# Performance work log

Measured on AMD Instinct MI355X. Metric: run time of the kernel, lower is better.

Reference implementation:

```python
import jax, jax.numpy as jnp
import numpy as np

# Sizes (match init_kwargs / input_specs)
N, D, H, E = 4096, 512, 2048, 8   # tokens, dim, hidden_dim, num_experts
DK = 2                             # dynamic_k = top_k(3) - fixed_k(1)
NC = E - 1                         # dynamic candidate count (experts 1..7)
BETA_FIXED = 1.0 / 3.0             # fixed_k / top_k
BETA_DYN = 2.0 / 3.0               # dynamic_k / top_k


def setup_inputs() -> dict:
    key = jax.random.key(0)
    ks = jax.random.split(key, 5)
    def init(k, shape, fan_in):
        return jax.random.normal(k, shape, jnp.float32) * (1.0 / np.sqrt(fan_in))
    return {
        "x": jax.random.normal(ks[0], (N, D), jnp.float32),
        "router_W": init(ks[1], (D, NC), D),      # Linear(dim, num_non_fixed)
        "router_b": jnp.zeros((NC,), jnp.float32),
        "W1": init(ks[2], (E, D, H), D),           # per-expert first Linear
        "b1": jnp.zeros((E, H), jnp.float32),
        "W2": init(ks[3], (E, H, D), H),           # per-expert second Linear
        "b2": jnp.zeros((E, D), jnp.float32),
        "fixed_w": jnp.ones((1,), jnp.float32),    # fixed_branch_weights
    }


def reference(x, router_W, router_b, W1, b1, W2, b2, fixed_w):
    # All-expert MLP computed once (dense grouped-GEMM form of the
    # per-expert gather/MLP/scatter loop in the torch module).
    h = jax.nn.relu(jnp.einsum("nd,edh->neh", x, W1) + b1)   # [N,E,H]
    y = jnp.einsum("neh,ehd->ned", h, W2) + b2               # [N,E,D]

    # Fixed branch: expert 0 with fixed weight.
    fixed_out = fixed_w[0] * y[:, 0]                          # [N,D]

    # Dynamic branch: router over the 7 non-fixed experts.
    logits = x @ router_W + router_b                          # [N,NC]
    top_logits, top_idx = jax.lax.top_k(logits, DK)           # [N,DK]
    gates = jax.nn.softmax(top_logits, axis=-1)               # [N,DK]
    sel_expert = top_idx + 1                                  # lookup non_fixed [1..7]

    # combine weights per (token, expert): scatter gates via one-hot.
    combine = jnp.sum(jax.nn.one_hot(sel_expert, E, dtype=x.dtype)
                      * gates[..., None], axis=1)             # [N,E]
    dyn_out = jnp.einsum("ned,ne->nd", y, combine)            # [N,D]

    mixed = BETA_FIXED * fixed_out + BETA_DYN * dyn_out

    # Aux losses (same math as torch).
    importance = jax.nn.softmax(logits, axis=-1).mean(axis=0)  # [NC]
    uniform = 1.0 / NC
    load_balance_loss = jnp.mean((importance - uniform) ** 2)
    router_entropy = -jnp.sum(importance * jnp.log(jnp.clip(importance, 1e-8)))

    return mixed, load_balance_loss, router_entropy, sel_expert
```

## Files before the change

### kernel.cpp

```cpp
#include <hip/hip_runtime.h>
#include <math.h>

#define N_TOK 4096
#define DIM   512
#define HID   2048
#define NEXP  8
#define NC    7
#define OUT_MIXED (N_TOK*DIM)
#define TM    48
#define TPE   86

typedef __attribute__((ext_vector_type(8))) short bf16x8;
typedef __attribute__((ext_vector_type(4))) float f32x4;

#define XSP 520
#define HSP 136

#define OFF_TOK  4096ull
#define OFF_WT   (OFF_TOK + 131072ull)
#define OFF_XBF  (OFF_WT + 131072ull)
#define OFF_W1S  (OFF_XBF + 4194304ull)
#define OFF_W2S  (OFF_W1S + 16777216ull)
#define WS_REQ   (OFF_W2S + 16777216ull)

__device__ inline unsigned short f2bf(float f) {
  unsigned int u = __builtin_bit_cast(unsigned int, f);
  u = (u + 0x7fffu + ((u >> 16) & 1u)) >> 16;
  return (unsigned short)u;
}

__device__ void dev_convert_w(const float* __restrict__ W,
                              unsigned int* __restrict__ Ws,
                              int K, int Nm, int tiles_n, int b,
                              unsigned short (*lds)[264])
{
  const int tid = threadIdx.x;
  const int e  = b >> 7;
  const int rm = b & 127;
  const int tk = rm / tiles_n;
  const int tn = rm - tk * tiles_n;

  const float* src = W + ((size_t)e * K + tk * 32) * Nm + tn * 256;
#pragma unroll
  for (int it = 0; it < 8; ++it) {
    const int g   = it * 256 + tid;
    const int row = g >> 6, c4 = g & 63;
    const float4 v = *(const float4*)(src + (size_t)row * Nm + c4 * 4);
    ushort4 o;
    o.x = f2bf(v.x); o.y = f2bf(v.y); o.z = f2bf(v.z); o.w = f2bf(v.w);
    *(ushort4*)(&lds[row][c4 * 4]) = o;
  }
  __syncthreads();

  const int ntiles = Nm >> 4, kblks = K >> 3;
#pragma unroll
  for (int it = 0; it < 16; ++it) {
    const int uid   = it * 256 + tid;
    const int nt_l  = uid >> 8;
    const int r     = uid & 255;
    const int kb_l  = r >> 6;
    const int u     = r & 63;
    const int n_lo  = u >> 2;
    const int k_hf  = u & 3;
    const int d_l   = kb_l * 8 + k_hf * 2;
    const int h_l   = nt_l * 16 + n_lo;
    const unsigned int s0 = lds[d_l][h_l], s1 = lds[d_l + 1][h_l];
    const int nt_g = tn * 16 + nt_l;
    const int kb_g = tk * 4 + kb_l;
    const size_t frag = ((size_t)e * ntiles + nt_g) * kblks + kb_g;
    Ws[frag * 64 + n_lo * 4 + k_hf] = s0 | (s1 << 16);
  }
}

__global__ __launch_bounds__(256) void prep_kernel(
    const float* __restrict__ x, const float* __restrict__ rW,
    const float* __restrict__ rb,
    const float* __restrict__ W1, const float* __restrict__ W2,
    float* __restrict__ out,
    int* __restrict__ cpad, float* __restrict__ ipad, int* __restrict__ done,
    int* __restrict__ tok_list, float* __restrict__ wt_list,
    unsigned short* __restrict__ xbf,
    unsigned int* __restrict__ W1s, unsigned int* __restrict__ W2s)
{
  __shared__ unsigned short clds[32][264];
  __shared__ float imp_loc[8];
  __shared__ int   cnt_loc[8];
  __shared__ int   ltok[8][32];
  __shared__ float lwt[8][32];
  __shared__ int   base_s[8];

  const int tid = threadIdx.x;
  const int blk = blockIdx.x;

  if (blk >= 256) {
    const int b = blk - 256;
    if (b < 512) {
      float* p = out + ((size_t)b * 256 + tid) * 16;
      const float4 z = {0.f, 0.f, 0.f, 0.f};
      *(float4*)(p)      = z;  *(float4*)(p + 4)  = z;
      *(float4*)(p + 8)  = z;  *(float4*)(p + 12) = z;
    } else if (b < 1536) {
      const int g = (b - 512) * 256 + tid;
      const float* src = x + (size_t)g * 8;
      unsigned short tmp[8];
#pragma unroll
      for (int j = 0; j < 8; ++j) tmp[j] = f2bf(src[j]);
      *(uint4*)(xbf + (size_t)g * 8) = *(const uint4*)tmp;
    } else if (b < 2560) {
      dev_convert_w(W1, W1s, DIM, HID, 8, b - 1536, clds);
    } else {
      dev_convert_w(W2, W2s, HID, DIM, 2, b - 2560, clds);
    }
    return;
  }

  if (tid < 8) { imp_loc[tid] = 0.f; cnt_loc[tid] = 0; }
  __syncthreads();
  const int wave = tid >> 6, lane = tid & 63;

  float rw[2][4][NC];
#pragma unroll
  for (int j = 0; j < 2; ++j) {
    const float* p = rW + j * 1792 + lane * 28;
    float tmp[28];
#pragma unroll
    for (int u = 0; u < 7; ++u) *(float4*)(tmp + u * 4) = *(const float4*)(p + u * 4);
#pragma unroll
    for (int k = 0; k < 4; ++k)
#pragma unroll
      for (int e = 0; e < NC; ++e) rw[j][k][e] = tmp[k * 7 + e];
  }

  for (int it = 0; it < 4; ++it) {
    const int t = blk * 16 + wave * 4 + it;
    const float4 xa = *(const float4*)(x + (size_t)t * DIM + lane * 4);
    const float4 xb = *(const float4*)(x + (size_t)t * DIM + 256 + lane * 4);
    const float xv[2][4] = {{xa.x, xa.y, xa.z, xa.w}, {xb.x, xb.y, xb.z, xb.w}};
    float lg[NC];
#pragma unroll
    for (int e = 0; e < NC; ++e) {
      float s = 0.f;
#pragma unroll
      for (int j = 0; j < 2; ++j)
#pragma unroll
        for (int k = 0; k < 4; ++k) s += xv[j][k] * rw[j][k][e];
      lg[e] = s;
    }
#pragma unroll
    for (int e = 0; e < NC; ++e) {
      float s = lg[e];
#pragma unroll
      for (int off = 32; off > 0; off >>= 1) s += __shfl_xor(s, off, 64);
      lg[e] = s + rb[e];
    }
    int i1 = 0; float l1 = lg[0];
#pragma unroll
    for (int e = 1; e < NC; ++e) { if (lg[e] > l1) { l1 = lg[e]; i1 = e; } }
    int i2 = -1; float l2 = -3.4e38f;
#pragma unroll
    for (int e = 0; e < NC; ++e) { if (e != i1 && lg[e] > l2) { l2 = lg[e]; i2 = e; } }

    const float ed = expf(l2 - l1);
    const float g1 = 1.f/(1.f+ed), g2 = ed/(1.f+ed);

    float p[NC]; float ssum = 0.f;
#pragma unroll
    for (int e = 0; e < NC; ++e) { p[e] = expf(lg[e] - l1); ssum += p[e]; }
    const float inv = 1.f/ssum;

    if (lane == 0) {
#pragma unroll
      for (int e = 0; e < NC; ++e) atomicAdd(&imp_loc[e], p[e]*inv);
      out[OUT_MIXED + 2 + 2*t]     = (float)(i1 + 1);
      out[OUT_MIXED + 2 + 2*t + 1] = (float)(i2 + 1);
      const int e1 = i1 + 1, e2 = i2 + 1;
      int p1 = atomicAdd(&cnt_loc[e1], 1);
      ltok[e1][p1] = t;  lwt[e1][p1] = (2.f/3.f)*g1;
      int p2 = atomicAdd(&cnt_loc[e2], 1);
      ltok[e2][p2] = t;  lwt[e2][p2] = (2.f/3.f)*g2;
    }
  }
  __syncthreads();

  if (tid >= 1 && tid < 8)
    base_s[tid] = atomicAdd(&cpad[tid * 32], cnt_loc[tid]);
  if (tid < NC)
    atomicAdd(&ipad[(tid + 1) * 32], imp_loc[tid]);
  __syncthreads();

  {
    const int e = tid >> 5, i = tid & 31;
    if (e >= 1 && i < cnt_loc[e]) {
      const int dst = e * N_TOK + base_s[e] + i;
      tok_list[dst] = ltok[e][i];
      wt_list [dst] = lwt[e][i];
    }
  }

  if (tid == 0) {
    __threadfence();
    const int old = atomicAdd(done, 1);
    if (old == 255) {
      __threadfence();
      float lb = 0.f, ent = 0.f;
      for (int e = 0; e < NC; ++e) {
        float p = ipad[(e + 1) * 32] * (1.f/(float)N_TOK);
        float d = p - (1.f/(float)NC);
        lb += d*d;
        ent -= p * logf(fmaxf(p, 1e-8f));
      }
      out[OUT_MIXED]     = lb * (1.f/(float)NC);
      out[OUT_MIXED + 1] = ent;
    }
  }
}

__global__ __launch_bounds__(512, 4) void moe_mlp_mfma(
    const unsigned short* __restrict__ xbf,
    const unsigned short* __restrict__ W1s,
    const unsigned short* __restrict__ W2s,
    const float* __restrict__ b1, const float* __restrict__ b2,
    const float* __restrict__ fixed_w,
    const int* __restrict__ cpad, const int* __restrict__ tok_list,
    const float* __restrict__ wt_list, float* __restrict__ out)
{
  const int e    = blockIdx.x / (TPE * 2);
  const int r    = blockIdx.x % (TPE * 2);
  const int tile = r >> 1;
  const int half = r & 1;
  const int cnt  = (e == 0) ? N_TOK : cpad[e * 32];
  const int start = tile * TM;
  if (start >= cnt) return;

  __shared__ __align__(16) unsigned short xs[TM * XSP];
  __shared__ __align__(16) unsigned short hs[TM * HSP];
  __shared__ int   tok_s[TM];
  __shared__ float wt_s[TM];

  const int tid = threadIdx.x;
  if (tid < TM) {
    int idx = start + tid; int t = 0; float w = 0.f;
    if (idx < cnt) {
      if (e == 0) { t = idx; w = (1.f/3.f) * fixed_w[0]; }
      else        { t = tok_list[e*N_TOK + idx]; w = wt_list[e*N_TOK + idx]; }
    }
    tok_s[tid] = t; wt_s[tid] = w;
  }
  __syncthreads();

  for (int i = tid; i < TM * 64; i += 512) {
    const int m = i >> 6, cb = i & 63;
    *(uint4*)(xs + m * XSP + cb * 8) =
        *(const uint4*)(xbf + (size_t)tok_s[m] * DIM + cb * 8);
  }

  const int lane = tid & 63;
  const int w    = tid >> 6;
  const int l15  = lane & 15;
  const int q    = lane >> 4;

  const unsigned short* W1e = W1s + (size_t)e * 128 * 64 * 128;
  const unsigned short* W2e = W2s + (size_t)e * 32 * 256 * 128;

  f32x4 yacc[3][4];
#pragma unroll
  for (int mi = 0; mi < 3; ++mi)
#pragma unroll
    for (int t = 0; t < 4; ++t) yacc[mi][t] = (f32x4){0.f, 0.f, 0.f, 0.f};

  __syncthreads();

  for (int c = half * 8; c < half * 8 + 8; ++c) {
    const int nt = c * 8 + w;
    f32x4 hacc[3];
#pragma unroll
    for (int mi = 0; mi < 3; ++mi) hacc[mi] = (f32x4){0.f, 0.f, 0.f, 0.f};
#pragma unroll 4
    for (int s = 0; s < 16; ++s) {
      const bf16x8 a0 = *(const bf16x8*)(xs + l15 * XSP + s * 32 + q * 8);
      const bf16x8 a1 = *(const bf16x8*)(xs + (16 + l15) * XSP + s * 32 + q * 8);
      const bf16x8 a2 = *(const bf16x8*)(xs + (32 + l15) * XSP + s * 32 + q * 8);
      const bf16x8 b = *(const bf16x8*)(
          W1e + ((size_t)nt * 64 + s * 4 + q) * 128 + l15 * 8);
      hacc[0] = __builtin_amdgcn_mfma_f32_16x16x32_bf16(a0, b, hacc[0], 0, 0, 0);
      hacc[1] = __builtin_amdgcn_mfma_f32_16x16x32_bf16(a1, b, hacc[1], 0, 0, 0);
      hacc[2] = __builtin_amdgcn_mfma_f32_16x16x32_bf16(a2, b, hacc[2], 0, 0, 0);
    }
    {
      const float bv = b1[e * HID + nt * 16 + l15];
      const int col = w * 16 + l15;
#pragma unroll
      for (int mi = 0; mi < 3; ++mi)
#pragma unroll
        for (int reg = 0; reg < 4; ++reg)
          hs[(mi * 16 + q * 4 + reg) * HSP + col] =
              f2bf(fmaxf(hacc[mi][reg] + bv, 0.f));
    }
    __syncthreads();

#pragma unroll
    for (int s = 0; s < 4; ++s) {
      const bf16x8 a0 = *(const bf16x8*)(hs + l15 * HSP + s * 32 + q * 8);
      const bf16x8 a1 = *(const bf16x8*)(hs + (16 + l15) * HSP + s * 32 + q * 8);
      const bf16x8 a2 = *(const bf16x8*)(hs + (32 + l15) * HSP + s * 32 + q * 8);
      const int kblk = c * 16 + s * 4 + q;
#pragma unroll
      for (int t = 0; t < 4; ++t) {
        const bf16x8 b = *(const bf16x8*)(
            W2e + (((size_t)(w * 4 + t) * 256) + kblk) * 128 + l15 * 8);
        yacc[0][t] = __builtin_amdgcn_mfma_f32_16x16x32_bf16(a0, b, yacc[0][t], 0, 0, 0);
        yacc[1][t] = __builtin_amdgcn_mfma_f32_16x16x32_bf16(a1, b, yacc[1][t], 0, 0, 0);
        yacc[2][t] = __builtin_amdgcn_mfma_f32_16x16x32_bf16(a2, b, yacc[2][t], 0, 0, 0);
      }
    }
    __syncthreads();
  }

#pragma unroll
  for (int t = 0; t < 4; ++t) {
    const int d = (w * 4 + t) * 16 + l15;
    const float b2v = half ? 0.f : b2[e * DIM + d];
#pragma unroll
    for (int mi = 0; mi < 3; ++mi)
#pragma unroll
      for (int reg = 0; reg < 4; ++reg) {
        const int m = mi * 16 + q * 4 + reg;
        atomicAdd(&out[(size_t)tok_s[m] * DIM + d], wt_s[m] * (yacc[mi][t][reg] + b2v));
      }
  }
}

__global__ __launch_bounds__(256) void router_only(
    const float* __restrict__ x, const float* __restrict__ rW,
    const float* __restrict__ rb, float* __restrict__ out,
    int* __restrict__ cpad, float* __restrict__ ipad, int* __restrict__ done,
    int* __restrict__ tok_list, float* __restrict__ wt_list)
{
  __shared__ float imp_loc[8];
  __shared__ int   cnt_loc[8];
  __shared__ int   ltok[8][32];
  __shared__ float lwt[8][32];
  __shared__ int   base_s[8];

  const int tid = threadIdx.x;
  if (tid < 8) { imp_loc[tid] = 0.f; cnt_loc[tid] = 0; }
  __syncthreads();
  const int wave = tid >> 6, lane = tid & 63;

  for (int it = 0; it < 4; ++it) {
    const int t = blockIdx.x * 16 + wave * 4 + it;
    float xv[8];
#pragma unroll
    for (int j = 0; j < 8; ++j) xv[j] = x[(size_t)t*DIM + lane + 64*j];
    float lg[NC];
#pragma unroll
    for (int e = 0; e < NC; ++e) {
      float s = 0.f;
#pragma unroll
      for (int j = 0; j < 8; ++j) s += xv[j] * rW[(lane + 64*j)*NC + e];
      lg[e] = s;
    }
#pragma unroll
    for (int e = 0; e < NC; ++e) {
      float s = lg[e];
#pragma unroll
      for (int off = 32; off > 0; off >>= 1) s += __shfl_xor(s, off, 64);
      lg[e] = s + rb[e];
    }
    int i1 = 0; float l1 = lg[0];
#pragma unroll
    for (int e = 1; e < NC; ++e) { if (lg[e] > l1) { l1 = lg[e]; i1 = e; } }
    int i2 = -1; float l2 = -3.4e38f;
#pragma unroll
    for (int e = 0; e < NC; ++e) { if (e != i1 && lg[e] > l2) { l2 = lg[e]; i2 = e; } }
    const float ed = expf(l2 - l1);
    const float g1 = 1.f/(1.f+ed), g2 = ed/(1.f+ed);
    float p[NC]; float ssum = 0.f;
#pragma unroll
    for (int e = 0; e < NC; ++e) { p[e] = expf(lg[e] - l1); ssum += p[e]; }
    const float inv = 1.f/ssum;
    if (lane == 0) {
#pragma unroll
      for (int e = 0; e < NC; ++e) atomicAdd(&imp_loc[e], p[e]*inv);
      out[OUT_MIXED + 2 + 2*t]     = (float)(i1 + 1);
      out[OUT_MIXED + 2 + 2*t + 1] = (float)(i2 + 1);
      const int e1 = i1 + 1, e2 = i2 + 1;
      int p1 = atomicAdd(&cnt_loc[e1], 1);
      ltok[e1][p1] = t;  lwt[e1][p1] = (2.f/3.f)*g1;
      int p2 = atomicAdd(&cnt_loc[e2], 1);
      ltok[e2][p2] = t;  lwt[e2][p2] = (2.f/3.f)*g2;
    }
  }
  __syncthreads();
  if (tid >= 1 && tid < 8)
    base_s[tid] = atomicAdd(&cpad[tid * 32], cnt_loc[tid]);
  if (tid < NC)
    atomicAdd(&ipad[(tid + 1) * 32], imp_loc[tid]);
  __syncthreads();
  {
    const int e = tid >> 5, i = tid & 31;
    if (e >= 1 && i < cnt_loc[e]) {
      const int dst = e * N_TOK + base_s[e] + i;
      tok_list[dst] = ltok[e][i];
      wt_list [dst] = lwt[e][i];
    }
  }
  if (tid == 0) {
    __threadfence();
    const int old = atomicAdd(done, 1);
    if (old == 255) {
      __threadfence();
      float lb = 0.f, ent = 0.f;
      for (int e = 0; e < NC; ++e) {
        float p = ipad[(e + 1) * 32] * (1.f/(float)N_TOK);
        float d = p - (1.f/(float)NC);
        lb += d*d;
        ent -= p * logf(fmaxf(p, 1e-8f));
      }
      out[OUT_MIXED]     = lb * (1.f/(float)NC);
      out[OUT_MIXED + 1] = ent;
    }
  }
}

__global__ __launch_bounds__(256) void moe_mlp_kernel(
    const float* __restrict__ x,
    const float* __restrict__ W1, const float* __restrict__ b1,
    const float* __restrict__ W2, const float* __restrict__ b2,
    const float* __restrict__ fixed_w,
    const int* __restrict__ cpad, const int* __restrict__ tok_list,
    const float* __restrict__ wt_list, float* __restrict__ out)
{
  const int e    = blockIdx.x >> 8;
  const int tile = blockIdx.x & 255;
  const int cnt  = (e == 0) ? N_TOK : cpad[e * 32];
  const int start = tile * 16;
  if (start >= cnt) return;

  __shared__ float xs[DIM][17];
  __shared__ float hs2[256][17];
  __shared__ int   tok_s[16];
  __shared__ float wt_s[16];

  const int tid = threadIdx.x;
  if (tid < 16) {
    int idx = start + tid; int t = 0; float w = 0.f;
    if (idx < cnt) {
      if (e == 0) { t = idx; w = (1.f/3.f) * fixed_w[0]; }
      else        { t = tok_list[e*N_TOK + idx]; w = wt_list[e*N_TOK + idx]; }
    }
    tok_s[tid] = t; wt_s[tid] = w;
  }
  __syncthreads();

  for (int i = tid; i < 16*DIM; i += 256) {
    const int m = i >> 9, d = i & (DIM-1);
    xs[d][m] = x[(size_t)tok_s[m]*DIM + d];
  }

  const int r  = tid & 63;
  const int m0 = (tid >> 6) * 4;
  const float* W1e = W1 + (size_t)e * DIM * HID;
  const float* W2e = W2 + (size_t)e * HID * DIM;
  const float* b1e = b1 + e * HID;

  float yacc[4][8];
#pragma unroll
  for (int j = 0; j < 4; ++j)
#pragma unroll
    for (int i = 0; i < 8; ++i) yacc[j][i] = 0.f;

  __syncthreads();

  for (int c = 0; c < 8; ++c) {
    const int k0 = c * 256;
    float bv[4];
#pragma unroll
    for (int i = 0; i < 4; ++i) bv[i] = b1e[k0 + r + 64*i];
    float hacc[4][4];
#pragma unroll
    for (int j = 0; j < 4; ++j)
#pragma unroll
      for (int i = 0; i < 4; ++i) hacc[j][i] = bv[i];
#pragma unroll 2
    for (int d = 0; d < DIM; ++d) {
      float wv[4];
#pragma unroll
      for (int i = 0; i < 4; ++i) wv[i] = W1e[(size_t)d*HID + k0 + r + 64*i];
      float xv[4];
#pragma unroll
      for (int j = 0; j < 4; ++j) xv[j] = xs[d][m0+j];
#pragma unroll
      for (int j = 0; j < 4; ++j)
#pragma unroll
        for (int i = 0; i < 4; ++i) hacc[j][i] += xv[j]*wv[i];
    }
#pragma unroll
    for (int i = 0; i < 4; ++i)
#pragma unroll
      for (int j = 0; j < 4; ++j) hs2[r + 64*i][m0+j] = fmaxf(hacc[j][i], 0.f);
    __syncthreads();

#pragma unroll 2
    for (int k = 0; k < 256; ++k) {
      float wv2[8];
#pragma unroll
      for (int i = 0; i < 8; ++i) wv2[i] = W2e[(size_t)(k0+k)*DIM + r + 64*i];
      float hv[4];
#pragma unroll
      for (int j = 0; j < 4; ++j) hv[j] = hs2[k][m0+j];
#pragma unroll
      for (int j = 0; j < 4; ++j)
#pragma unroll
        for (int i = 0; i < 8; ++i) yacc[j][i] += hv[j]*wv2[i];
    }
    __syncthreads();
  }

#pragma unroll
  for (int i = 0; i < 8; ++i) {
    const int d = r + 64*i;
    const float b2v = b2[e*DIM + d];
#pragma unroll
    for (int j = 0; j < 4; ++j) {
      const int m = m0 + j;
      atomicAdd(&out[(size_t)tok_s[m]*DIM + d], wt_s[m]*(yacc[j][i] + b2v));
    }
  }
}

extern "C" void kernel_launch(void* const* d_in, const int* in_sizes, int n_in,
                              void* d_out, int out_size, void* d_ws, size_t ws_size,
                              hipStream_t stream)
{
  const float* x  = (const float*)d_in[0];
  const float* rW = (const float*)d_in[1];
  const float* rb = (const float*)d_in[2];
  const float* W1 = (const float*)d_in[3];
  const float* b1 = (const float*)d_in[4];
  const float* W2 = (const float*)d_in[5];
  const float* b2 = (const float*)d_in[6];
  const float* fw = (const float*)d_in[7];
  float* out = (float*)d_out;

  int*   cpad     = (int*)d_ws;
  float* ipad     = (float*)((char*)d_ws + 1024);
  int*   done     = (int*)((char*)d_ws + 2048);
  int*   tok_list = (int*)((char*)d_ws + OFF_TOK);
  float* wt_list  = (float*)((char*)d_ws + OFF_WT);

  hipMemsetAsync(d_ws, 0, 4096, stream);

  if (ws_size >= WS_REQ) {
    unsigned short* xbf = (unsigned short*)((char*)d_ws + OFF_XBF);
    unsigned int*   W1s = (unsigned int*)((char*)d_ws + OFF_W1S);
    unsigned int*   W2s = (unsigned int*)((char*)d_ws + OFF_W2S);
    prep_kernel<<<3840, 256, 0, stream>>>(x, rW, rb, W1, W2, out,
                                          cpad, ipad, done, tok_list, wt_list,
                                          xbf, W1s, W2s);
    moe_mlp_mfma<<<NEXP*TPE*2, 512, 0, stream>>>(xbf, (const unsigned short*)W1s,
                                                 (const unsigned short*)W2s, b1, b2, fw,
                                                 cpad, tok_list, wt_list, out);
  } else {
    hipMemsetAsync(d_out, 0, (size_t)OUT_MIXED*4, stream);
    router_only<<<256, 256, 0, stream>>>(x, rW, rb, out, cpad, ipad, done,
                                         tok_list, wt_list);
    moe_mlp_kernel<<<NEXP*256, 256, 0, stream>>>(x, W1, b1, W2, b2, fw,
                                                 cpad, tok_list, wt_list, out);
  }
}
```

Before: 288.0 us.

## Shrink token tile to 32 and widen hidden chunk with prefetched weight loads

The token tile drops from 48 to 32 rows and each block now processes 256-wide hidden chunks, with each wave owning two 16-column tiles. W1 and W2 fragments are software-prefetched from global memory a few k-steps ahead so loads overlap the MFMA work. The grid becomes 256 blocks per expert and the launch bound is raised to 6 blocks per CU for occupancy. In exchange, each weight fragment is reused across fewer token rows, so global weight traffic per token goes up, and the larger register and LDS footprint may limit occupancy.

```diff
diff --git a/kernel.cpp b/kernel.cpp
--- a/kernel.cpp
+++ b/kernel.cpp
@@ -7,14 +7,13 @@
 #define NEXP  8
 #define NC    7
 #define OUT_MIXED (N_TOK*DIM)
-#define TM    48
-#define TPE   86
+#define TM    32
 
 typedef __attribute__((ext_vector_type(8))) short bf16x8;
 typedef __attribute__((ext_vector_type(4))) float f32x4;
 
 #define XSP 520
-#define HSP 136
+#define HSP 264
 
 #define OFF_TOK  4096ull
 #define OFF_WT   (OFF_TOK + 131072ull)
@@ -215,7 +214,7 @@
   }
 }
 
-__global__ __launch_bounds__(512, 4) void moe_mlp_mfma(
+__global__ __launch_bounds__(512, 6) void moe_mlp_mfma(
     const unsigned short* __restrict__ xbf,
     const unsigned short* __restrict__ W1s,
     const unsigned short* __restrict__ W2s,
@@ -224,10 +223,10 @@
     const int* __restrict__ cpad, const int* __restrict__ tok_list,
     const float* __restrict__ wt_list, float* __restrict__ out)
 {
-  const int e    = blockIdx.x / (TPE * 2);
-  const int r    = blockIdx.x % (TPE * 2);
-  const int tile = r >> 1;
-  const int half = r & 1;
+  const int e    = blockIdx.x >> 8;
+  const int rest = blockIdx.x & 255;
+  const int tile = rest >> 1;
+  const int half = rest & 1;
   const int cnt  = (e == 0) ? N_TOK : cpad[e * 32];
   const int start = tile * TM;
   if (start >= cnt) return;
@@ -262,71 +261,94 @@
   const unsigned short* W1e = W1s + (size_t)e * 128 * 64 * 128;
   const unsigned short* W2e = W2s + (size_t)e * 32 * 256 * 128;
 
-  f32x4 yacc[3][4];
-#pragma unroll
-  for (int mi = 0; mi < 3; ++mi)
+#define B1LD(s,t) (*(const bf16x8*)(W1e + (((size_t)(nt_base + (t)) * 64) + (s) * 4 + q) * 128 + l15 * 8))
+#define B2LD(s,t) (*(const bf16x8*)(W2e + (((size_t)(w * 4 + (t)) * 256) + c * 32 + (s) * 4 + q) * 128 + l15 * 8))
+
+  f32x4 yacc[2][4];
+#pragma unroll
+  for (int mi = 0; mi < 2; ++mi)
 #pragma unroll
     for (int t = 0; t < 4; ++t) yacc[mi][t] = (f32x4){0.f, 0.f, 0.f, 0.f};
 
   __syncthreads();
 
-  for (int c = half * 8; c < half * 8 + 8; ++c) {
-    const int nt = c * 8 + w;
-    f32x4 hacc[3];
-#pragma unroll
-    for (int mi = 0; mi < 3; ++mi) hacc[mi] = (f32x4){0.f, 0.f, 0.f, 0.f};
-#pragma unroll 4
+  for (int c = half * 4; c < half * 4 + 4; ++c) {
+    const int nt_base = c * 16 + w * 2;
+    f32x4 hacc[2][2];
+#pragma unroll
+    for (int mi = 0; mi < 2; ++mi)
+#pragma unroll
+      for (int t = 0; t < 2; ++t) hacc[mi][t] = (f32x4){0.f, 0.f, 0.f, 0.f};
+
+    bf16x8 bb0[2], bb1[2];
+    bb0[0] = B1LD(0, 0); bb0[1] = B1LD(0, 1);
+    bb1[0] = B1LD(1, 0); bb1[1] = B1LD(1, 1);
+#pragma unroll
     for (int s = 0; s < 16; ++s) {
+      const int sp = (s + 2 < 16) ? s + 2 : 15;
+      const bf16x8 nb0 = B1LD(sp, 0);
+      const bf16x8 nb1 = B1LD(sp, 1);
       const bf16x8 a0 = *(const bf16x8*)(xs + l15 * XSP + s * 32 + q * 8);
       const bf16x8 a1 = *(const bf16x8*)(xs + (16 + l15) * XSP + s * 32 + q * 8);
-      const bf16x8 a2 = *(const bf16x8*)(xs + (32 + l15) * XSP + s * 32 + q * 8);
-      const bf16x8 b = *(const bf16x8*)(
-          W1e + ((size_t)nt * 64 + s * 4 + q) * 128 + l15 * 8);
-      hacc[0] = __builtin_amdgcn_mfma_f32_16x16x32_bf16(a0, b, hacc[0], 0, 0, 0);
-      hacc[1] = __builtin_amdgcn_mfma_f32_16x16x32_bf16(a1, b, hacc[1], 0, 0, 0);
-      hacc[2] = __builtin_amdgcn_mfma_f32_16x16x32_bf16(a2, b, hacc[2], 0, 0, 0);
-    }
-    {
-      const float bv = b1[e * HID + nt * 16 + l15];
-      const int col = w * 16 + l15;
-#pragma unroll
-      for (int mi = 0; mi < 3; ++mi)
-#pragma unroll
-        for (int reg = 0; reg < 4; ++reg)
-          hs[(mi * 16 + q * 4 + reg) * HSP + col] =
-              f2bf(fmaxf(hacc[mi][reg] + bv, 0.f));
+      const bf16x8 c0 = (s & 1) ? bb1[0] : bb0[0];
+      const bf16x8 c1 = (s & 1) ? bb1[1] : bb0[1];
+      hacc[0][0] = __builtin_amdgcn_mfma_f32_16x16x32_bf16(a0, c0, hacc[0][0], 0, 0, 0);
+      hacc[1][0] = __builtin_amdgcn_mfma_f32_16x16x32_bf16(a1, c0, hacc[1][0], 0, 0, 0);
+      hacc[0][1] = __builtin_amdgcn_mfma_f32_16x16x32_bf16(a0, c1, hacc[0][1], 0, 0, 0);
+      hacc[1][1] = __builtin_amdgcn_mfma_f32_16x16x32_bf16(a1, c1, hacc[1][1], 0, 0, 0);
+      if (s & 1) { bb1[0] = nb0; bb1[1] = nb1; }
+      else       { bb0[0] = nb0; bb0[1] = nb1; }
+    }
+
+#pragma unroll
+    for (int t = 0; t < 2; ++t) {
+      const float bv = b1[e * HID + (nt_base + t) * 16 + l15];
+      const int col = w * 32 + t * 16 + l15;
+#pragma unroll
+      for (int reg = 0; reg < 4; ++reg) {
+        hs[(q * 4 + reg) * HSP + col]      = f2bf(fmaxf(hacc[0][t][reg] + bv, 0.f));
+        hs[(16 + q * 4 + reg) * HSP + col] = f2bf(fmaxf(hacc[1][t][reg] + bv, 0.f));
+      }
     }
     __syncthreads();
 
-#pragma unroll
-    for (int s = 0; s < 4; ++s) {
+    bf16x8 cur[4];
+#pragma unroll
+    for (int t = 0; t < 4; ++t) cur[t] = B2LD(0, t);
+#pragma unroll
+    for (int s = 0; s < 8; ++s) {
+      const int sp = (s + 1 < 8) ? s + 1 : 7;
+      const bf16x8 n0 = B2LD(sp, 0);
+      const bf16x8 n1 = B2LD(sp, 1);
+      const bf16x8 n2 = B2LD(sp, 2);
+      const bf16x8 n3 = B2LD(sp, 3);
       const bf16x8 a0 = *(const bf16x8*)(hs + l15 * HSP + s * 32 + q * 8);
       const bf16x8 a1 = *(const bf16x8*)(hs + (16 + l15) * HSP + s * 32 + q * 8);
-      const bf16x8 a2 = *(const bf16x8*)(hs + (32 + l15) * HSP + s * 32 + q * 8);
-      const int kblk = c * 16 + s * 4 + q;
-#pragma unroll
-      for (int t = 0; t < 4; ++t) {
-        const bf16x8 b = *(const bf16x8*)(
-            W2e + (((size_t)(w * 4 + t) * 256) + kblk) * 128 + l15 * 8);
-        yacc[0][t] = __builtin_amdgcn_mfma_f32_16x16x32_bf16(a0, b, yacc[0][t], 0, 0, 0);
-        yacc[1][t] = __builtin_amdgcn_mfma_f32_16x16x32_bf16(a1, b, yacc[1][t], 0, 0, 0);
-        yacc[2][t] = __builtin_amdgcn_mfma_f32_16x16x32_bf16(a2, b, yacc[2][t], 0, 0, 0);
-      }
+      yacc[0][0] = __builtin_amdgcn_mfma_f32_16x16x32_bf16(a0, cur[0], yacc[0][0], 0, 0, 0);
+      yacc[1][0] = __builtin_amdgcn_mfma_f32_16x16x32_bf16(a1, cur[0], yacc[1][0], 0, 0, 0);
+      yacc[0][1] = __builtin_amdgcn_mfma_f32_16x16x32_bf16(a0, cur[1], yacc[0][1], 0, 0, 0);
+      yacc[1][1] = __builtin_amdgcn_mfma_f32_16x16x32_bf16(a1, cur[1], yacc[1][1], 0, 0, 0);
+      yacc[0][2] = __builtin_amdgcn_mfma_f32_16x16x32_bf16(a0, cur[2], yacc[0][2], 0, 0, 0);
+      yacc[1][2] = __builtin_amdgcn_mfma_f32_16x16x32_bf16(a1, cur[2], yacc[1][2], 0, 0, 0);
+      yacc[0][3] = __builtin_amdgcn_mfma_f32_16x16x32_bf16(a0, cur[3], yacc[0][3], 0, 0, 0);
+      yacc[1][3] = __builtin_amdgcn_mfma_f32_16x16x32_bf16(a1, cur[3], yacc[1][3], 0, 0, 0);
+      cur[0] = n0; cur[1] = n1; cur[2] = n2; cur[3] = n3;
     }
     __syncthreads();
   }
+#undef B1LD
+#undef B2LD
 
 #pragma unroll
   for (int t = 0; t < 4; ++t) {
     const int d = (w * 4 + t) * 16 + l15;
     const float b2v = half ? 0.f : b2[e * DIM + d];
 #pragma unroll
-    for (int mi = 0; mi < 3; ++mi)
-#pragma unroll
-      for (int reg = 0; reg < 4; ++reg) {
-        const int m = mi * 16 + q * 4 + reg;
-        atomicAdd(&out[(size_t)tok_s[m] * DIM + d], wt_s[m] * (yacc[mi][t][reg] + b2v));
-      }
+    for (int reg = 0; reg < 4; ++reg) {
+      const int m0 = q * 4 + reg, m1 = 16 + q * 4 + reg;
+      atomicAdd(&out[(size_t)tok_s[m0] * DIM + d], wt_s[m0] * (yacc[0][t][reg] + b2v));
+      atomicAdd(&out[(size_t)tok_s[m1] * DIM + d], wt_s[m1] * (yacc[1][t][reg] + b2v));
+    }
   }
 }
 
@@ -558,9 +580,9 @@
     prep_kernel<<<3840, 256, 0, stream>>>(x, rW, rb, W1, W2, out,
                                           cpad, ipad, done, tok_list, wt_list,
                                           xbf, W1s, W2s);
-    moe_mlp_mfma<<<NEXP*TPE*2, 512, 0, stream>>>(xbf, (const unsigned short*)W1s,
-                                                 (const unsigned short*)W2s, b1, b2, fw,
-                                                 cpad, tok_list, wt_list, out);
+    moe_mlp_mfma<<<NEXP*256, 512, 0, stream>>>(xbf, (const unsigned short*)W1s,
+                                               (const unsigned short*)W2s, b1, b2, fw,
+                                               cpad, tok_list, wt_list, out);
   } else {
     hipMemsetAsync(d_out, 0, (size_t)OUT_MIXED*4, stream);
     router_only<<<256, 256, 0, stream>>>(x, rW, rb, out, cpad, ipad, done,
```

New measurement: 342.6 us. 19.0% more time.
